# Kernel tuning notes

Hardware: AMD Instinct MI355X
Metric: run time of the kernel (lower is better)

## Reference

```python
import jax, jax.numpy as jnp
import numpy as np

H, KV, D = 12, 4, 128  # n_head, n_kv_head, head_dim
VE_GATE_CH = 12

def _rmsnorm(x):
    eps = jnp.finfo(x.dtype).eps  # matches torch F.rms_norm default eps
    return x * jax.lax.rsqrt(jnp.mean(x * x, axis=-1, keepdims=True) + eps)

def _rope(x, cos, sin):
    d = x.shape[-1] // 2
    x1, x2 = x[..., :d], x[..., d:]
    return jnp.concatenate([x1 * cos + x2 * sin, -x1 * sin + x2 * cos], axis=-1)

def setup_inputs() -> dict:
    key = jax.random.key(0)
    ks = jax.random.split(key, 9)
    B, T, C = 2, 2048, 1536
    x = jax.random.normal(ks[0], (B, T, C), jnp.float32)
    ve = jax.random.normal(ks[1], (B, T, KV * D), jnp.float32)
    ang = jax.random.uniform(ks[2], (1, T, 1, D // 2), jnp.float32) * (2.0 * np.pi)
    cos, sin = jnp.cos(ang), jnp.sin(ang)
    Wq = jax.random.normal(ks[3], (H * D, C), jnp.float32) * 0.02
    Wk = jax.random.normal(ks[4], (KV * D, C), jnp.float32) * 0.02
    Wv = jax.random.normal(ks[5], (KV * D, C), jnp.float32) * 0.02
    Wproj = jax.random.normal(ks[6], (C, C), jnp.float32) * 0.02
    Wg = jax.random.normal(ks[7], (KV, VE_GATE_CH), jnp.float32) * 0.02
    return dict(x=x, ve=ve, cos=cos, sin=sin, Wq=Wq, Wk=Wk, Wv=Wv, Wproj=Wproj, Wg=Wg, window=1024)

def reference(x, ve, cos, sin, Wq, Wk, Wv, Wproj, Wg, window):
    B, T, C = x.shape
    q = (x @ Wq.T).reshape(B, T, H, D)
    k = (x @ Wk.T).reshape(B, T, KV, D)
    v = (x @ Wv.T).reshape(B, T, KV, D)
    # value-embedding gate: 3*sigmoid(Linear(x[..., :12])) per kv head
    gate = 3.0 * jax.nn.sigmoid(x[..., :VE_GATE_CH] @ Wg.T)  # [B,T,KV]
    v = v + gate[..., None] * ve.reshape(B, T, KV, D)
    q = _rmsnorm(_rope(q, cos, sin)) * 1.2
    k = _rmsnorm(_rope(k, cos, sin)) * 1.2
    rep = H // KV  # GQA group size
    qh = q.transpose(0, 2, 1, 3).reshape(B, KV, rep, T, D)
    kh = k.transpose(0, 2, 1, 3)  # [B,KV,T,D]
    vh = v.transpose(0, 2, 1, 3)
    scores = jnp.einsum('bgrtd,bgsd->bgrts', qh, kh) / np.sqrt(D)
    row = jnp.arange(T)[:, None]
    col = jnp.arange(T)[None, :]
    if window < 0 or window >= T:
        mask = col <= row  # pure causal
    else:
        mask = (col <= row) & (row - col <= window)  # causal sliding window
    scores = jnp.where(mask, scores, -jnp.inf)
    att = jax.nn.softmax(scores, axis=-1)
    y = jnp.einsum('bgrts,bgsd->bgrtd', att, vh)
    y = y.reshape(B, H, T, D).transpose(0, 2, 1, 3).reshape(B, T, H * D)
    return y @ Wproj.T
```

## Files before the change

kernel.cpp:

```cpp
#include <hip/hip_runtime.h>
#include <hip/hip_bf16.h>
#include <math.h>

#define B_  2
#define T_  2048
#define C_  1536
#define H_  12
#define KV_ 4
#define D_  128
#define M_  (B_*T_)
#define REP_ (H_/KV_)
#define NQKV_ 2560
#define KK_  1536
#define NKT_ 24

typedef __bf16 bf16x8 __attribute__((ext_vector_type(8)));
typedef float  f32x4  __attribute__((ext_vector_type(4)));
typedef unsigned u32x4 __attribute__((ext_vector_type(4)));

union BCast { u32x4 u; bf16x8 b; };

__device__ inline bf16x8 ldb8(const ushort* p) {
    BCast c; c.u = *reinterpret_cast<const u32x4*>(p); return c.b;
}

__device__ inline ushort f2bf(float f) {
    union { float f; unsigned u; } v; v.f = f;
    unsigned u = v.u;
    return (ushort)((u + 0x7FFF + ((u >> 16) & 1)) >> 16);
}

__device__ inline float bf2f(ushort u) {
    union { unsigned u; float f; } v; v.u = (unsigned)u << 16;
    return v.f;
}

__device__ inline void async_copy16(const ushort* g, ushort* l) {
    __builtin_amdgcn_global_load_lds(
        (const __attribute__((address_space(1))) unsigned*)g,
        (__attribute__((address_space(3))) unsigned*)l, 16, 0, 0);
}

__device__ __host__ inline int dperm(int d) {
    return (d < 32) ? d : (d < 64 ? d + 32 : (d < 96 ? d - 32 : d));
}

#define MFMA16(va, vb, d) d = __builtin_amdgcn_mfma_f32_16x16x32_bf16(va, vb, d, 0, 0, 0)

#define CLUSTER(AARR, BARR, MB, NB)                                        \
    __builtin_amdgcn_s_setprio(1);                                         \
    _Pragma("unroll")                                                      \
    for (int mf = 0; mf < 4; mf++)                                         \
        _Pragma("unroll")                                                  \
        for (int nf = 0; nf < 2; nf++) {                                   \
            MFMA16(AARR[mf*2+0], BARR[nf*2+0], acc[(MB)+mf][(NB)+nf]);     \
            MFMA16(AARR[mf*2+1], BARR[nf*2+1], acc[(MB)+mf][(NB)+nf]);     \
        }                                                                  \
    __builtin_amdgcn_s_setprio(0);

#define RD_AL(bo_) { _Pragma("unroll") for (int mf = 0; mf < 4; mf++) {    \
        aL[mf*2+0] = ldb8(aB0 + (bo_) + mf*1024);                          \
        aL[mf*2+1] = ldb8(aB1 + (bo_) + mf*1024); } }
#define RD_AH(bo_) { _Pragma("unroll") for (int mf = 0; mf < 4; mf++) {    \
        aH[mf*2+0] = ldb8(aB0 + (bo_) + 4096 + mf*1024);                   \
        aH[mf*2+1] = ldb8(aB1 + (bo_) + 4096 + mf*1024); } }
#define RD_B0(bo_) { _Pragma("unroll") for (int nf = 0; nf < 2; nf++) {    \
        b0[nf*2+0] = ldb8(bB0 + (bo_) + nf*1024);                          \
        b0[nf*2+1] = ldb8(bB1 + (bo_) + nf*1024); } }
#define RD_B1(bo_) { _Pragma("unroll") for (int nf = 0; nf < 2; nf++) {    \
        b1[nf*2+0] = ldb8(bB0 + (bo_) + 2048 + nf*1024);                   \
        b1[nf*2+1] = ldb8(bB1 + (bo_) + 2048 + nf*1024); } }

template<int EPI>
__global__ __launch_bounds__(512) void gemm256(const ushort* __restrict__ A,
                                               const ushort* __restrict__ Bm,
                                               ushort* __restrict__ Qp,
                                               ushort* __restrict__ Kp,
                                               ushort* __restrict__ vbuf,
                                               float* __restrict__ Cf,
                                               const float* __restrict__ cosb,
                                               const float* __restrict__ sinb) {
    __shared__ ushort lds[2][2][2][8192];
    const int tid  = threadIdx.x;
    const int wave = tid >> 6, lane = tid & 63;
    const int m16 = lane & 15, quad = lane >> 4;
    const int WM = wave >> 2, WN = wave & 3;
    const int brow = (WN & 1) << 6;

    const int nwg  = gridDim.x * gridDim.y;
    const int orig = blockIdx.y * gridDim.x + blockIdx.x;
    const int vid  = (orig & 7) * (nwg >> 3) + (orig >> 3);
    const int bxT  = vid >> 4;
    const int byT  = vid & 15;
    const int bm = byT << 8, bn = bxT << 8;

    const int r = tid >> 3;
    const int slot8 = ((tid & 7) ^ (r & 7)) << 3;
    const ushort* Ag = A  + (size_t)(bm + r) * KK_ + slot8;
    const ushort* Bg = Bm + (size_t)(bn + r) * KK_ + slot8;
    const size_t row64 = (size_t)64 * KK_;
    const size_t hskip = (size_t)128 * KK_;

    auto stage2 = [&](const ushort* Gp, int buf, int op, int kc) {
        ushort* base = &lds[0][0][0][0] + op * 32768 + buf * 16384 + wave * 512;
        const ushort* g = Gp + kc;
        async_copy16(g,                 base);
        async_copy16(g + row64,         base + 4096);
        async_copy16(g + hskip,         base + 8192);
        async_copy16(g + hskip + row64, base + 8192 + 4096);
    };

    const int swzu = (m16 & 7) << 3;
    const int k0u  = (quad * 8) ^ swzu;
    const int k1u  = (32 + quad * 8) ^ swzu;
    const ushort* ldsu = &lds[0][0][0][0];
    const ushort* aB0 = ldsu + (WM ? 8192 : 0) + (m16 << 6) + k0u;
    const ushort* aB1 = ldsu + (WM ? 8192 : 0) + (m16 << 6) + k1u;
    const ushort* bB0 = ldsu + 32768 + ((WN >> 1) ? 8192 : 0) + ((brow + m16) << 6) + k0u;
    const ushort* bB1 = ldsu + 32768 + ((WN >> 1) ? 8192 : 0) + ((brow + m16) << 6) + k1u;

    f32x4 acc[8][4];
    #pragma unroll
    for (int i = 0; i < 8; i++)
        #pragma unroll
        for (int j = 0; j < 4; j++) acc[i][j] = (f32x4){0.f, 0.f, 0.f, 0.f};

    stage2(Bg, 0, 1, 0);  stage2(Ag, 0, 0, 0);
    stage2(Bg, 1, 1, 64); stage2(Ag, 1, 0, 64);
    __builtin_amdgcn_s_waitcnt(0x0F78);
    __builtin_amdgcn_sched_barrier(0);
    __builtin_amdgcn_s_barrier();
    __builtin_amdgcn_sched_barrier(0);

    #pragma unroll 1
    for (int kt = 0; kt < NKT_; kt++) {
        const int bo = (kt & 1) ? 16384 : 0;
        bf16x8 aL[8], aH[8], b0[4], b1[4];
        RD_AL(bo); RD_B0(bo); RD_B1(bo); RD_AH(bo);
        CLUSTER(aL, b0, 0, 0);
        __builtin_amdgcn_s_barrier();
        CLUSTER(aL, b1, 0, 2);
        __builtin_amdgcn_s_barrier();
        CLUSTER(aH, b1, 4, 2);
        __builtin_amdgcn_s_barrier();
        CLUSTER(aH, b0, 4, 0);
        if (kt < NKT_ - 1) {
            __builtin_amdgcn_sched_barrier(0);
            __builtin_amdgcn_s_barrier();
            __builtin_amdgcn_sched_barrier(0);
            if (kt < NKT_ - 2) {
                stage2(Bg, kt & 1, 1, (kt + 2) << 6);
                stage2(Ag, kt & 1, 0, (kt + 2) << 6);
                __builtin_amdgcn_s_waitcnt(0x0F78);
            } else {
                __builtin_amdgcn_s_waitcnt(0x0F70);
            }
            __builtin_amdgcn_sched_barrier(0);
            __builtin_amdgcn_s_barrier();
            __builtin_amdgcn_sched_barrier(0);
        }
    }
    __syncthreads();

    if constexpr (EPI == 0) {
        if (bn >= 2048) {
            const int cb = bn - 2048 + WN*64;
            #pragma unroll
            for (int m = 0; m < 8; m++) {
                const int rl = WM*128 + (m>>2)*64 + (m&3)*16 + quad*4;
                #pragma unroll
                for (int reg = 0; reg < 4; reg++) {
                    ushort* vr = vbuf + (size_t)(bm + rl + reg) * 512 + cb + m16;
                    #pragma unroll
                    for (int j = 0; j < 4; j++)
                        vr[(j>>1)*32 + (j&1)*16] = f2bf(acc[m][j][reg]);
                }
            }
        } else {
            float* ssqS = (float*)&lds[0][0][0][0];
            #pragma unroll
            for (int m = 0; m < 8; m++) {
                #pragma unroll
                for (int reg = 0; reg < 4; reg++) {
                    float v = acc[m][0][reg]*acc[m][0][reg] + acc[m][1][reg]*acc[m][1][reg]
                            + acc[m][2][reg]*acc[m][2][reg] + acc[m][3][reg]*acc[m][3][reg];
                    v += __shfl_xor(v, 1); v += __shfl_xor(v, 2);
                    v += __shfl_xor(v, 4); v += __shfl_xor(v, 8);
                    if (m16 == 0) {
                        const int rl = WM*128 + (m>>2)*64 + (m&3)*16 + quad*4 + reg;
                        ssqS[rl*4 + WN] = v;
                    }
                }
            }
            __syncthreads();

            const bool isq = (bn < 1536);
            const float osc = isq ? (1.2f * 1.2f * 0.08838834764831845f) : 1.0f;
            const int hh = (isq ? (bn >> 7) : ((bn - 1536) >> 7)) + (WN >> 1);
            const int nh  = isq ? H_ : KV_;
            ushort* outp  = isq ? Qp : Kp;

            #pragma unroll
            for (int m = 0; m < 8; m++) {
                #pragma unroll
                for (int reg = 0; reg < 4; reg++) {
                    const int rl = WM*128 + (m>>2)*64 + (m&3)*16 + quad*4 + reg;
                    const int row = bm + rl;
                    const float tot = ssqS[rl*4 + (WN & ~1)] + ssqS[rl*4 + (WN | 1)];
                    const float sc = rsqrtf(tot * (1.0f/128.0f) + 1.1920928955078125e-07f) * osc;
                    const int b = row >> 11, t = row & (T_ - 1);
                    ushort* orow = outp + ((size_t)(b * nh + hh) * T_ + t) * D_;
                    #pragma unroll
                    for (int nf = 0; nf < 2; nf++) {
                        const int ipair = (WN & 1) * 32 + nf*16 + m16;
                        const float c = cosb[t*64 + ipair], s = sinb[t*64 + ipair];
                        const float x1 = acc[m][nf][reg], x2 = acc[m][2+nf][reg];
                        const int oc = (WN & 1) * 64 + nf*16 + m16;
                        orow[oc]      = f2bf((x1*c + x2*s) * sc);
                        orow[oc + 32] = f2bf((x2*c - x1*s) * sc);
                    }
                }
            }
        }
    } else {
        #pragma unroll
        for (int m = 0; m < 8; m++) {
            const int rl = WM*128 + (m>>2)*64 + (m&3)*16 + quad*4;
            #pragma unroll
            for (int reg = 0; reg < 4; reg++) {
                float* cr = Cf + (size_t)(bm + rl + reg) * C_ + bn + WN*64 + m16;
                #pragma unroll
                for (int j = 0; j < 4; j++)
                    cr[(j>>1)*32 + (j&1)*16] = acc[m][j][reg];
            }
        }
    }
}

#define SEG0 1572864
#define SEG1 2162688
#define SEG2 2359296
#define SEG3 2555904
#define SEG4 3145728
#define ROW4 384
__global__ __launch_bounds__(256) void cast_all(const float* __restrict__ x,
                                                const float* __restrict__ Wq,
                                                const float* __restrict__ Wk,
                                                const float* __restrict__ Wv,
                                                const float* __restrict__ Wp,
                                                ushort* __restrict__ xb,
                                                ushort* __restrict__ Wqkvb,
                                                ushort* __restrict__ Wpb) {
    const int i = blockIdx.x * 256 + threadIdx.x;
    float4 v; size_t dst4; ushort* dstp;
    if (i < SEG0) {
        v = ((const float4*)x)[i]; dstp = xb; dst4 = i;
    } else if (i < SEG1) {
        const int j = i - SEG0;
        const int r = j / ROW4, c4 = j - r * ROW4;
        const int d = r & 127, hh = r >> 7;
        v = ((const float4*)Wq)[j]; dstp = Wqkvb;
        dst4 = (size_t)(hh * 128 + dperm(d)) * ROW4 + c4;
    } else if (i < SEG2) {
        const int j = i - SEG1;
        const int r = j / ROW4, c4 = j - r * ROW4;
        const int d = r & 127, g = r >> 7;
        v = ((const float4*)Wk)[j]; dstp = Wqkvb;
        dst4 = (size_t)(1536 + g * 128 + dperm(d)) * ROW4 + c4;
    } else if (i < SEG3) {
        const int j = i - SEG2;
        v = ((const float4*)Wv)[j]; dstp = Wqkvb;
        dst4 = (size_t)2048 * ROW4 + j;
    } else {
        const int j = i - SEG3;
        v = ((const float4*)Wp)[j]; dstp = Wpb; dst4 = j;
    }
    ((ushort4*)dstp)[dst4] = make_ushort4(f2bf(v.x), f2bf(v.y), f2bf(v.z), f2bf(v.w));
}

__global__ __launch_bounds__(256) void gate_vt(const ushort* __restrict__ vbuf,
                                               const float* __restrict__ x,
                                               const float* __restrict__ ve,
                                               const float* __restrict__ Wg,
                                               ushort* __restrict__ Vt) {
    const int t0 = blockIdx.x * 64, g = blockIdx.y, b = blockIdx.z;
    __shared__ float gateS[64];
    __shared__ ushort tile[128][66];
    const int tid = threadIdx.x;
    if (tid < 64) {
        const float* xr = x + (size_t)(b * T_ + t0 + tid) * C_;
        float acc = 0.f;
        #pragma unroll
        for (int c = 0; c < 12; c++) acc += xr[c] * Wg[g * 12 + c];
        gateS[tid] = 3.0f / (1.0f + __expf(-acc));
    }
    __syncthreads();
    #pragma unroll
    for (int i = 0; i < 32; i++) {
        int idx = i * 256 + tid;
        int r = idx >> 7;
        int d = idx & 127;
        size_t offv = (size_t)(b * T_ + t0 + r) * 512 + g * D_ + d;
        tile[d][r] = f2bf(bf2f(vbuf[offv]) + gateS[r] * ve[offv]);
    }
    __syncthreads();
    ushort* ob = Vt + ((size_t)(b * KV_ + g) * D_) * T_ + t0;
    #pragma unroll
    for (int i = 0; i < 32; i++) {
        int idx = i * 256 + tid;
        int d = idx >> 6;
        int c = idx & 63;
        ob[(size_t)d * T_ + c] = tile[d][c];
    }
}

__global__ __launch_bounds__(256, 3) void attn_mfma(const ushort* __restrict__ Qp,
                                                    const ushort* __restrict__ Kp,
                                                    const ushort* __restrict__ Vt,
                                                    ushort* __restrict__ Y,
                                                    const int* __restrict__ wptr) {
    const int t0 = blockIdx.x * 64;
    const int h  = blockIdx.y, b = blockIdx.z;
    const int g  = h / REP_;
    const int tid  = threadIdx.x;
    const int wave = tid >> 6, lane = tid & 63;
    const int m16 = lane & 15, quad = lane >> 4;

    __shared__ ushort Ks[4 * 32 * 32];
    __shared__ ushort Vs[128 * 32];
    __shared__ ushort Pl[4][16 * 40];

    const int w = *wptr;
    const bool windowed = (w >= 0 && w < T_);
    const unsigned wu = windowed ? (unsigned)w : 0x7FFFFFFFu;
    int s_lo = 0;
    if (windowed) { s_lo = t0 - w; if (s_lo < 0) s_lo = 0; }
    const int s_hi = t0 + 63;
    const int ss0 = s_lo & ~31;
    const int tw = t0 + wave * 16;

    const ushort* qrow = Qp + ((size_t)(b * H_ + h) * T_ + tw + m16) * D_ + quad * 8;
    bf16x8 qa[4];
    #pragma unroll
    for (int kc = 0; kc < 4; kc++) qa[kc] = ldb8(qrow + kc * 32);

    const ushort* kbase = Kp + (size_t)(b * KV_ + g) * T_ * D_;
    const ushort* vbase = Vt + (size_t)(b * KV_ + g) * D_ * T_;

    const int c0 = wave, c1 = wave + 4;
    const ushort* kg0 = kbase + (size_t)((c0 & 1) * 16 + (lane >> 2)) * D_ + (c0 >> 1) * 32 + (lane & 3) * 8;
    const ushort* kg1 = kbase + (size_t)((c1 & 1) * 16 + (lane >> 2)) * D_ + (c1 >> 1) * 32 + (lane & 3) * 8;
    ushort* kl0 = Ks + c0 * 512;
    ushort* kl1 = Ks + c1 * 512;
    const ushort* vg0 = vbase + (size_t)(c0 * 16 + (lane >> 2)) * T_ + (lane & 3) * 8;
    const ushort* vg1 = vbase + (size_t)(c1 * 16 + (lane >> 2)) * T_ + (lane & 3) * 8;
    ushort* vl0 = Vs + c0 * 512;
    ushort* vl1 = Vs + c1 * 512;

    f32x4 o[8];
    #pragma unroll
    for (int dt = 0; dt < 8; dt++) o[dt] = (f32x4){0.f, 0.f, 0.f, 0.f};
    f32x4 lacc = (f32x4){0.f, 0.f, 0.f, 0.f};
    BCast onesc; onesc.u = (u32x4){0x3F803F80u, 0x3F803F80u, 0x3F803F80u, 0x3F803F80u};
    const bf16x8 ones = onesc.b;
    ushort* pw = &Pl[wave][0];

    for (int ss = ss0; ss <= s_hi; ss += 32) {
        const size_t koff = (size_t)ss * D_;
        async_copy16(kg0 + koff, kl0);
        async_copy16(kg1 + koff, kl1);
        async_copy16(vg0 + ss,   vl0);
        async_copy16(vg1 + ss,   vl1);
        __syncthreads();

        f32x4 s0 = (f32x4){0.f,0.f,0.f,0.f};
        f32x4 s1 = (f32x4){0.f,0.f,0.f,0.f};
        #pragma unroll
        for (int kc = 0; kc < 4; kc++) {
            bf16x8 kf0 = ldb8(Ks + kc * 1024 + m16 * 32 + quad * 8);
            bf16x8 kf1 = ldb8(Ks + kc * 1024 + (16 + m16) * 32 + quad * 8);
            s0 = __builtin_amdgcn_mfma_f32_16x16x32_bf16(qa[kc], kf0, s0, 0, 0, 0);
            s1 = __builtin_amdgcn_mfma_f32_16x16x32_bf16(qa[kc], kf1, s1, 0, 0, 0);
        }

        const int sA = ss + m16, sB = ss + 16 + m16;
        #pragma unroll
        for (int reg = 0; reg < 4; reg++) {
            const int t = tw + quad * 4 + reg;
            const float pa = ((unsigned)(t - sA) <= wu) ? __expf(s0[reg]) : 0.f;
            const float pb = ((unsigned)(t - sB) <= wu) ? __expf(s1[reg]) : 0.f;
            pw[(quad * 4 + reg) * 40 + m16]      = f2bf(pa);
            pw[(quad * 4 + reg) * 40 + 16 + m16] = f2bf(pb);
        }

        __builtin_amdgcn_s_waitcnt(0xc07f);
        bf16x8 pfrag = ldb8(pw + m16 * 40 + quad * 8);

        #pragma unroll
        for (int dt = 0; dt < 8; dt++) {
            bf16x8 vf = ldb8(Vs + (dt * 16 + m16) * 32 + quad * 8);
            o[dt] = __builtin_amdgcn_mfma_f32_16x16x32_bf16(pfrag, vf, o[dt], 0, 0, 0);
        }
        lacc = __builtin_amdgcn_mfma_f32_16x16x32_bf16(pfrag, ones, lacc, 0, 0, 0);
        __syncthreads();
    }

    float inv[4];
    #pragma unroll
    for (int reg = 0; reg < 4; reg++) inv[reg] = 1.0f / lacc[reg];
    ushort* yb = Y + ((size_t)(b * T_ + tw + quad * 4) * H_ + h) * D_ + m16;
    #pragma unroll
    for (int reg = 0; reg < 4; reg++)
        #pragma unroll
        for (int dt = 0; dt < 8; dt++)
            yb[(size_t)reg * H_ * D_ + dt * 16] = f2bf(o[dt][reg] * inv[reg]);
}

extern "C" void kernel_launch(void* const* d_in, const int* in_sizes, int n_in,
                              void* d_out, int out_size, void* d_ws, size_t ws_size,
                              hipStream_t stream) {
    const float* x     = (const float*)d_in[0];
    const float* ve    = (const float*)d_in[1];
    const float* cosb  = (const float*)d_in[2];
    const float* sinb  = (const float*)d_in[3];
    const float* Wq    = (const float*)d_in[4];
    const float* Wk    = (const float*)d_in[5];
    const float* Wv    = (const float*)d_in[6];
    const float* Wproj = (const float*)d_in[7];
    const float* Wg    = (const float*)d_in[8];
    const int*   wptr  = (const int*)d_in[9];
    float* out = (float*)d_out;

    ushort* xb    = (ushort*)d_ws;
    ushort* vbuf  = xb    + (size_t)M_ * C_;
    ushort* Qp    = vbuf  + (size_t)M_ * 512;
    ushort* Kp    = Qp    + (size_t)M_ * C_;
    ushort* Vt    = Kp    + (size_t)M_ * 512;
    ushort* yb16  = Vt    + (size_t)M_ * 512;
    ushort* Wqkvb = yb16  + (size_t)M_ * C_;
    ushort* Wpb   = Wqkvb + (size_t)NQKV_ * C_;

    cast_all<<<SEG4 / 256, 256, 0, stream>>>(x, Wq, Wk, Wv, Wproj, xb, Wqkvb, Wpb);

    gemm256<0><<<dim3(NQKV_ / 256, M_ / 256), 512, 0, stream>>>(
        xb, Wqkvb, Qp, Kp, vbuf, nullptr, cosb, sinb);

    gate_vt<<<dim3(T_ / 64, KV_, B_), 256, 0, stream>>>(vbuf, x, ve, Wg, Vt);

    attn_mfma<<<dim3(T_ / 64, H_, B_), 256, 0, stream>>>(Qp, Kp, Vt, yb16, wptr);

    gemm256<1><<<dim3(C_ / 256, M_ / 256), 512, 0, stream>>>(
        yb16, Wpb, nullptr, nullptr, nullptr, out, nullptr, nullptr);
}
```

Baseline: 269.3 us.

## Shrink GEMM tiles from 256x256 to 128x128 for more workgroups

Replaces the 512-thread 256x256-tile GEMM with a 256-thread 128x128-tile kernel running two workgroups per CU. The wave layout becomes 2x2 with 64x64 per wave, the clustered barrier-interleaved MFMA schedule is dropped, and the RMSNorm/RoPE and V epilogues are remapped to the new layout. The goal is better CU fill for the small projection GEMMs (the old grid gave only 160 and 96 workgroups), at the cost of less data reuse per tile and more global/LDS traffic.

```diff
diff --git a/kernel.cpp b/kernel.cpp
--- a/kernel.cpp
+++ b/kernel.cpp
@@ -47,86 +47,61 @@
 
 #define MFMA16(va, vb, d) d = __builtin_amdgcn_mfma_f32_16x16x32_bf16(va, vb, d, 0, 0, 0)
 
-#define CLUSTER(AARR, BARR, MB, NB)                                        \
-    __builtin_amdgcn_s_setprio(1);                                         \
-    _Pragma("unroll")                                                      \
-    for (int mf = 0; mf < 4; mf++)                                         \
-        _Pragma("unroll")                                                  \
-        for (int nf = 0; nf < 2; nf++) {                                   \
-            MFMA16(AARR[mf*2+0], BARR[nf*2+0], acc[(MB)+mf][(NB)+nf]);     \
-            MFMA16(AARR[mf*2+1], BARR[nf*2+1], acc[(MB)+mf][(NB)+nf]);     \
-        }                                                                  \
-    __builtin_amdgcn_s_setprio(0);
-
-#define RD_AL(bo_) { _Pragma("unroll") for (int mf = 0; mf < 4; mf++) {    \
-        aL[mf*2+0] = ldb8(aB0 + (bo_) + mf*1024);                          \
-        aL[mf*2+1] = ldb8(aB1 + (bo_) + mf*1024); } }
-#define RD_AH(bo_) { _Pragma("unroll") for (int mf = 0; mf < 4; mf++) {    \
-        aH[mf*2+0] = ldb8(aB0 + (bo_) + 4096 + mf*1024);                   \
-        aH[mf*2+1] = ldb8(aB1 + (bo_) + 4096 + mf*1024); } }
-#define RD_B0(bo_) { _Pragma("unroll") for (int nf = 0; nf < 2; nf++) {    \
-        b0[nf*2+0] = ldb8(bB0 + (bo_) + nf*1024);                          \
-        b0[nf*2+1] = ldb8(bB1 + (bo_) + nf*1024); } }
-#define RD_B1(bo_) { _Pragma("unroll") for (int nf = 0; nf < 2; nf++) {    \
-        b1[nf*2+0] = ldb8(bB0 + (bo_) + 2048 + nf*1024);                   \
-        b1[nf*2+1] = ldb8(bB1 + (bo_) + 2048 + nf*1024); } }
-
 template<int EPI>
-__global__ __launch_bounds__(512) void gemm256(const ushort* __restrict__ A,
-                                               const ushort* __restrict__ Bm,
-                                               ushort* __restrict__ Qp,
-                                               ushort* __restrict__ Kp,
-                                               ushort* __restrict__ vbuf,
-                                               float* __restrict__ Cf,
-                                               const float* __restrict__ cosb,
-                                               const float* __restrict__ sinb) {
-    __shared__ ushort lds[2][2][2][8192];
+__global__ __launch_bounds__(256, 2) void gemm128(const ushort* __restrict__ A,
+                                                  const ushort* __restrict__ Bm,
+                                                  ushort* __restrict__ Qp,
+                                                  ushort* __restrict__ Kp,
+                                                  ushort* __restrict__ vbuf,
+                                                  float* __restrict__ Cf,
+                                                  const float* __restrict__ cosb,
+                                                  const float* __restrict__ sinb) {
+    __shared__ ushort ldsA[2][8192];
+    __shared__ ushort ldsB[2][8192];
     const int tid  = threadIdx.x;
     const int wave = tid >> 6, lane = tid & 63;
     const int m16 = lane & 15, quad = lane >> 4;
-    const int WM = wave >> 2, WN = wave & 3;
-    const int brow = (WN & 1) << 6;
+    const int WM = wave >> 1, WN = wave & 1;
 
     const int nwg  = gridDim.x * gridDim.y;
     const int orig = blockIdx.y * gridDim.x + blockIdx.x;
     const int vid  = (orig & 7) * (nwg >> 3) + (orig >> 3);
-    const int bxT  = vid >> 4;
-    const int byT  = vid & 15;
-    const int bm = byT << 8, bn = bxT << 8;
+    const int gy   = gridDim.y;
+    const int bxT  = vid / gy;
+    const int byT  = vid - bxT * gy;
+    const int bm = byT << 7, bn = bxT << 7;
 
     const int r = tid >> 3;
     const int slot8 = ((tid & 7) ^ (r & 7)) << 3;
     const ushort* Ag = A  + (size_t)(bm + r) * KK_ + slot8;
     const ushort* Bg = Bm + (size_t)(bn + r) * KK_ + slot8;
-    const size_t row64 = (size_t)64 * KK_;
-    const size_t hskip = (size_t)128 * KK_;
-
-    auto stage2 = [&](const ushort* Gp, int buf, int op, int kc) {
-        ushort* base = &lds[0][0][0][0] + op * 32768 + buf * 16384 + wave * 512;
+    const size_t row32 = (size_t)32 * KK_;
+
+    auto stage = [&](const ushort* Gp, ushort* ldsOp, int kc) {
+        ushort* base = ldsOp + wave * 512;
         const ushort* g = Gp + kc;
-        async_copy16(g,                 base);
-        async_copy16(g + row64,         base + 4096);
-        async_copy16(g + hskip,         base + 8192);
-        async_copy16(g + hskip + row64, base + 8192 + 4096);
+        async_copy16(g,             base);
+        async_copy16(g +   row32,   base + 2048);
+        async_copy16(g + 2*row32,   base + 4096);
+        async_copy16(g + 3*row32,   base + 6144);
     };
 
     const int swzu = (m16 & 7) << 3;
     const int k0u  = (quad * 8) ^ swzu;
     const int k1u  = (32 + quad * 8) ^ swzu;
-    const ushort* ldsu = &lds[0][0][0][0];
-    const ushort* aB0 = ldsu + (WM ? 8192 : 0) + (m16 << 6) + k0u;
-    const ushort* aB1 = ldsu + (WM ? 8192 : 0) + (m16 << 6) + k1u;
-    const ushort* bB0 = ldsu + 32768 + ((WN >> 1) ? 8192 : 0) + ((brow + m16) << 6) + k0u;
-    const ushort* bB1 = ldsu + 32768 + ((WN >> 1) ? 8192 : 0) + ((brow + m16) << 6) + k1u;
-
-    f32x4 acc[8][4];
-    #pragma unroll
-    for (int i = 0; i < 8; i++)
+    const ushort* aB0 = &ldsA[0][0] + ((WM * 64 + m16) << 6) + k0u;
+    const ushort* aB1 = &ldsA[0][0] + ((WM * 64 + m16) << 6) + k1u;
+    const ushort* bB0 = &ldsB[0][0] + ((WN * 64 + m16) << 6) + k0u;
+    const ushort* bB1 = &ldsB[0][0] + ((WN * 64 + m16) << 6) + k1u;
+
+    f32x4 acc[4][4];
+    #pragma unroll
+    for (int i = 0; i < 4; i++)
         #pragma unroll
         for (int j = 0; j < 4; j++) acc[i][j] = (f32x4){0.f, 0.f, 0.f, 0.f};
 
-    stage2(Bg, 0, 1, 0);  stage2(Ag, 0, 0, 0);
-    stage2(Bg, 1, 1, 64); stage2(Ag, 1, 0, 64);
+    stage(Bg, ldsB[0], 0);  stage(Ag, ldsA[0], 0);
+    stage(Bg, ldsB[1], 64); stage(Ag, ldsA[1], 64);
     __builtin_amdgcn_s_waitcnt(0x0F78);
     __builtin_amdgcn_sched_barrier(0);
     __builtin_amdgcn_s_barrier();
@@ -134,23 +109,34 @@
 
     #pragma unroll 1
     for (int kt = 0; kt < NKT_; kt++) {
-        const int bo = (kt & 1) ? 16384 : 0;
-        bf16x8 aL[8], aH[8], b0[4], b1[4];
-        RD_AL(bo); RD_B0(bo); RD_B1(bo); RD_AH(bo);
-        CLUSTER(aL, b0, 0, 0);
-        __builtin_amdgcn_s_barrier();
-        CLUSTER(aL, b1, 0, 2);
-        __builtin_amdgcn_s_barrier();
-        CLUSTER(aH, b1, 4, 2);
-        __builtin_amdgcn_s_barrier();
-        CLUSTER(aH, b0, 4, 0);
+        const int bo = (kt & 1) ? 8192 : 0;
+        bf16x8 a[8], b[8];
+        #pragma unroll
+        for (int mf = 0; mf < 4; mf++) {
+            a[mf*2+0] = ldb8(aB0 + bo + mf*1024);
+            a[mf*2+1] = ldb8(aB1 + bo + mf*1024);
+        }
+        #pragma unroll
+        for (int nf = 0; nf < 4; nf++) {
+            b[nf*2+0] = ldb8(bB0 + bo + nf*1024);
+            b[nf*2+1] = ldb8(bB1 + bo + nf*1024);
+        }
+        __builtin_amdgcn_s_setprio(1);
+        #pragma unroll
+        for (int mf = 0; mf < 4; mf++)
+            #pragma unroll
+            for (int nf = 0; nf < 4; nf++) {
+                MFMA16(a[mf*2+0], b[nf*2+0], acc[mf][nf]);
+                MFMA16(a[mf*2+1], b[nf*2+1], acc[mf][nf]);
+            }
+        __builtin_amdgcn_s_setprio(0);
         if (kt < NKT_ - 1) {
             __builtin_amdgcn_sched_barrier(0);
             __builtin_amdgcn_s_barrier();
             __builtin_amdgcn_sched_barrier(0);
             if (kt < NKT_ - 2) {
-                stage2(Bg, kt & 1, 1, (kt + 2) << 6);
-                stage2(Ag, kt & 1, 0, (kt + 2) << 6);
+                stage(Bg, ldsB[kt & 1], (kt + 2) << 6);
+                stage(Ag, ldsA[kt & 1], (kt + 2) << 6);
                 __builtin_amdgcn_s_waitcnt(0x0F78);
             } else {
                 __builtin_amdgcn_s_waitcnt(0x0F70);
@@ -164,31 +150,31 @@
 
     if constexpr (EPI == 0) {
         if (bn >= 2048) {
-            const int cb = bn - 2048 + WN*64;
+            const int cb = bn - 2048 + WN * 64;
             #pragma unroll
-            for (int m = 0; m < 8; m++) {
-                const int rl = WM*128 + (m>>2)*64 + (m&3)*16 + quad*4;
+            for (int mf = 0; mf < 4; mf++) {
+                const int rl = WM*64 + mf*16 + quad*4;
                 #pragma unroll
                 for (int reg = 0; reg < 4; reg++) {
                     ushort* vr = vbuf + (size_t)(bm + rl + reg) * 512 + cb + m16;
                     #pragma unroll
-                    for (int j = 0; j < 4; j++)
-                        vr[(j>>1)*32 + (j&1)*16] = f2bf(acc[m][j][reg]);
+                    for (int nf = 0; nf < 4; nf++)
+                        vr[nf*16] = f2bf(acc[mf][nf][reg]);
                 }
             }
         } else {
-            float* ssqS = (float*)&lds[0][0][0][0];
+            float* ssqS = (float*)&ldsA[0][0];
             #pragma unroll
-            for (int m = 0; m < 8; m++) {
+            for (int mf = 0; mf < 4; mf++) {
                 #pragma unroll
                 for (int reg = 0; reg < 4; reg++) {
-                    float v = acc[m][0][reg]*acc[m][0][reg] + acc[m][1][reg]*acc[m][1][reg]
-                            + acc[m][2][reg]*acc[m][2][reg] + acc[m][3][reg]*acc[m][3][reg];
+                    float v = acc[mf][0][reg]*acc[mf][0][reg] + acc[mf][1][reg]*acc[mf][1][reg]
+                            + acc[mf][2][reg]*acc[mf][2][reg] + acc[mf][3][reg]*acc[mf][3][reg];
                     v += __shfl_xor(v, 1); v += __shfl_xor(v, 2);
                     v += __shfl_xor(v, 4); v += __shfl_xor(v, 8);
                     if (m16 == 0) {
-                        const int rl = WM*128 + (m>>2)*64 + (m&3)*16 + quad*4 + reg;
-                        ssqS[rl*4 + WN] = v;
+                        const int rl = WM*64 + mf*16 + quad*4 + reg;
+                        ssqS[rl*2 + WN] = v;
                     }
                 }
             }
@@ -196,26 +182,26 @@
 
             const bool isq = (bn < 1536);
             const float osc = isq ? (1.2f * 1.2f * 0.08838834764831845f) : 1.0f;
-            const int hh = (isq ? (bn >> 7) : ((bn - 1536) >> 7)) + (WN >> 1);
+            const int hh  = isq ? (bn >> 7) : ((bn - 1536) >> 7);
             const int nh  = isq ? H_ : KV_;
             ushort* outp  = isq ? Qp : Kp;
 
             #pragma unroll
-            for (int m = 0; m < 8; m++) {
+            for (int mf = 0; mf < 4; mf++) {
                 #pragma unroll
                 for (int reg = 0; reg < 4; reg++) {
-                    const int rl = WM*128 + (m>>2)*64 + (m&3)*16 + quad*4 + reg;
+                    const int rl = WM*64 + mf*16 + quad*4 + reg;
                     const int row = bm + rl;
-                    const float tot = ssqS[rl*4 + (WN & ~1)] + ssqS[rl*4 + (WN | 1)];
+                    const float tot = ssqS[rl*2] + ssqS[rl*2 + 1];
                     const float sc = rsqrtf(tot * (1.0f/128.0f) + 1.1920928955078125e-07f) * osc;
                     const int b = row >> 11, t = row & (T_ - 1);
                     ushort* orow = outp + ((size_t)(b * nh + hh) * T_ + t) * D_;
                     #pragma unroll
                     for (int nf = 0; nf < 2; nf++) {
-                        const int ipair = (WN & 1) * 32 + nf*16 + m16;
+                        const int ipair = WN * 32 + nf*16 + m16;
                         const float c = cosb[t*64 + ipair], s = sinb[t*64 + ipair];
-                        const float x1 = acc[m][nf][reg], x2 = acc[m][2+nf][reg];
-                        const int oc = (WN & 1) * 64 + nf*16 + m16;
+                        const float x1 = acc[mf][nf][reg], x2 = acc[mf][nf+2][reg];
+                        const int oc = WN * 64 + nf*16 + m16;
                         orow[oc]      = f2bf((x1*c + x2*s) * sc);
                         orow[oc + 32] = f2bf((x2*c - x1*s) * sc);
                     }
@@ -224,14 +210,14 @@
         }
     } else {
         #pragma unroll
-        for (int m = 0; m < 8; m++) {
-            const int rl = WM*128 + (m>>2)*64 + (m&3)*16 + quad*4;
+        for (int mf = 0; mf < 4; mf++) {
+            const int rl = WM*64 + mf*16 + quad*4;
             #pragma unroll
             for (int reg = 0; reg < 4; reg++) {
                 float* cr = Cf + (size_t)(bm + rl + reg) * C_ + bn + WN*64 + m16;
                 #pragma unroll
-                for (int j = 0; j < 4; j++)
-                    cr[(j>>1)*32 + (j&1)*16] = acc[m][j][reg];
+                for (int nf = 0; nf < 4; nf++)
+                    cr[nf*16] = acc[mf][nf][reg];
             }
         }
     }
@@ -442,13 +428,13 @@
 
     cast_all<<<SEG4 / 256, 256, 0, stream>>>(x, Wq, Wk, Wv, Wproj, xb, Wqkvb, Wpb);
 
-    gemm256<0><<<dim3(NQKV_ / 256, M_ / 256), 512, 0, stream>>>(
+    gemm128<0><<<dim3(NQKV_ / 128, M_ / 128), 256, 0, stream>>>(
         xb, Wqkvb, Qp, Kp, vbuf, nullptr, cosb, sinb);
 
     gate_vt<<<dim3(T_ / 64, KV_, B_), 256, 0, stream>>>(vbuf, x, ve, Wg, Vt);
 
     attn_mfma<<<dim3(T_ / 64, H_, B_), 256, 0, stream>>>(Qp, Kp, Vt, yb16, wptr);
 
-    gemm256<1><<<dim3(C_ / 256, M_ / 256), 512, 0, stream>>>(
+    gemm128<1><<<dim3(C_ / 128, M_ / 128), 256, 0, stream>>>(
         yb16, Wpb, nullptr, nullptr, nullptr, out, nullptr, nullptr);
 }
```

Result: faster. 258.5 us (-4.0%).
